# Optimization experiments

Measured on AMD Instinct MI355X. Metric: run time of the kernel, lower is better.

## Reference

```python
import jax, jax.numpy as jnp
import numpy as np

# Mamba2 config (matches mamba_ssm.Mamba2 defaults used by the wrapper)
D_MODEL = 1024
D_STATE = 128
D_CONV = 4
EXPAND = 2
HEADDIM = 64
CHUNK = 256
D_INNER = EXPAND * D_MODEL            # 2048
NHEADS = D_INNER // HEADDIM           # 32
CONV_DIM = D_INNER + 2 * D_STATE      # 2304 (x, B, C share the causal conv)
D_IN_PROJ = 2 * D_INNER + 2 * D_STATE + NHEADS  # z, xBC, dt
EPS = 1e-5


def rmsnorm(x, w, eps=EPS):
    return x * jax.lax.rsqrt(jnp.mean(x * x, axis=-1, keepdims=True) + eps) * w


def setup_inputs() -> dict:
    key = jax.random.key(0)
    ks = jax.random.split(key, 8)
    B, L = 2, 2048
    def w(k, shape, sc=0.02):
        return jax.random.normal(k, shape, jnp.float32) * sc
    return {
        "x": jax.random.normal(ks[0], (B, L, D_MODEL), jnp.float32),
        "norm_w": jnp.ones((D_MODEL,), jnp.float32),
        "in_proj_w": w(ks[1], (D_IN_PROJ, D_MODEL)),
        "conv_w": w(ks[2], (CONV_DIM, 1, D_CONV), 0.2),   # depthwise kernel
        "conv_b": jnp.zeros((CONV_DIM,), jnp.float32),
        "dt_bias": w(ks[3], (NHEADS,), 1.0),
        "A_log": jnp.log(1.0 + 15.0 * jax.random.uniform(ks[4], (NHEADS,), jnp.float32)),
        "D": jnp.ones((NHEADS,), jnp.float32),
        "gnorm_w": jnp.ones((D_INNER,), jnp.float32),
        "out_proj_w": w(ks[5], (D_MODEL, D_INNER)),
    }


def _ssd(xd, a, Bm, Cm):
    """Chunked SSD scan (ssd_minimal_discrete).
    xd: (b,l,h,p) = x*dt ; a: (b,l,h) = dt*A ; Bm,Cm: (b,l,n) (ngroups=1)."""
    b, l, h, p = xd.shape
    n = Bm.shape[-1]
    nc = l // CHUNK
    xd = xd.reshape(b, nc, CHUNK, h, p)
    a = a.reshape(b, nc, CHUNK, h).transpose(0, 3, 1, 2)   # (b,h,nc,c)
    Bm = Bm.reshape(b, nc, CHUNK, n)
    Cm = Cm.reshape(b, nc, CHUNK, n)
    a_cs = jnp.cumsum(a, axis=-1)                           # (b,h,nc,c)
    # 1) intra-chunk: causal decay matrix L[t,s] = exp(sum_{s<i<=t} a_i)
    diff = a_cs[..., :, None] - a_cs[..., None, :]          # (b,h,nc,c,c)
    mask = jnp.tril(jnp.ones((CHUNK, CHUNK), bool))
    Lm = jnp.exp(jnp.where(mask, diff, 0.0)) * mask
    Y_diag = jnp.einsum("bcln,bcsn,bhcls,bcshp->bclhp", Cm, Bm, Lm, xd)
    # 2) per-chunk end states
    decay_states = jnp.exp(a_cs[..., -1:] - a_cs)           # (b,h,nc,c)
    states = jnp.einsum("bcln,bhcl,bclhp->bchpn", Bm, decay_states, xd)
    # 3) inter-chunk recurrence (vectorized segsum over the 8+1 chunk totals)
    tot = jnp.pad(a_cs[..., -1], ((0, 0), (0, 0), (1, 0)))  # (b,h,nc+1)
    tot_cs = jnp.cumsum(tot, axis=-1)
    dchunk = tot_cs[..., :, None] - tot_cs[..., None, :]    # (b,h,nc+1,nc+1)
    cmask = jnp.tril(jnp.ones((nc + 1, nc + 1), bool))
    dchunk = jnp.exp(jnp.where(cmask, dchunk, 0.0)) * cmask
    states = jnp.concatenate([jnp.zeros_like(states[:, :1]), states], axis=1)
    new_states = jnp.einsum("bhzc,bchpn->bzhpn", dchunk, states)
    init_states = new_states[:, :-1]                        # state entering each chunk
    # 4) state -> output contribution
    Y_off = jnp.einsum("bcln,bchpn,bhcl->bclhp", Cm, init_states, jnp.exp(a_cs))
    return (Y_diag + Y_off).reshape(b, l, h, p)


def reference(x, norm_w, in_proj_w, conv_w, conv_b, dt_bias, A_log, D, gnorm_w, out_proj_w):
    res = x
    u = rmsnorm(x, norm_w)
    zxbcdt = u @ in_proj_w.T                                # (b,l,d_in_proj)
    z, xBC, dt = jnp.split(zxbcdt, [D_INNER, D_INNER + CONV_DIM], axis=-1)
    # causal depthwise conv1d over (x,B,C), then SiLU
    xBC_t = jnp.pad(xBC.transpose(0, 2, 1), ((0, 0), (0, 0), (D_CONV - 1, 0)))
    conv = jax.lax.conv_general_dilated(
        xBC_t, conv_w, (1,), "VALID",
        dimension_numbers=("NCH", "OIH", "NCH"), feature_group_count=CONV_DIM)
    xBC = jax.nn.silu(conv.transpose(0, 2, 1) + conv_b)
    xs, Bm, Cm = jnp.split(xBC, [D_INNER, D_INNER + D_STATE], axis=-1)
    dt = jax.nn.softplus(dt + dt_bias)                      # (b,l,h)
    A = -jnp.exp(A_log)                                     # (h,)
    xh = xs.reshape(xs.shape[0], xs.shape[1], NHEADS, HEADDIM)
    y = _ssd(xh * dt[..., None], dt * A, Bm, Cm)
    y = y + D[None, None, :, None] * xh                     # skip term
    y = y.reshape(xs.shape)
    y = rmsnorm(y * jax.nn.silu(z), gnorm_w)                # gated RMSNorm
    return res + y @ out_proj_w.T
```

## Files before the change

### kernel.cpp

```cpp
#include <hip/hip_runtime.h>
#include <hip/hip_bf16.h>

typedef __hip_bfloat16 bf16_t;
typedef __attribute__((ext_vector_type(8))) short bfrag8;
typedef __attribute__((ext_vector_type(4))) float floatx4;

#define DM     1024
#define DI     2048
#define NHD    32
#define HD     64
#define DSTATE 128
#define CONVD  2304
#define NPROJ  4384
#define NPAD   4480
#define MR     4096
#define LL     2048
#define EPSF   1e-5f
#define LOG2E  1.44269504088896f

__device__ __forceinline__ void gl_lds16(const void* g, void* l) {
  __builtin_amdgcn_global_load_lds((const __attribute__((address_space(1))) void*)g,
                                   (__attribute__((address_space(3))) void*)l, 16, 0, 0);
}
__device__ __forceinline__ unsigned pack_bf16_rn(float a, float b) {
  unsigned ua = (__float_as_uint(a) + 0x8000u) >> 16;
  unsigned ub = (__float_as_uint(b) + 0x8000u) >> 16;
  return ua | (ub << 16);
}
__device__ __forceinline__ unsigned short bf16u(float a) {
  return (unsigned short)((__float_as_uint(a) + 0x8000u) >> 16);
}
__device__ __forceinline__ float blo(unsigned u){ return __uint_as_float(u << 16); }
__device__ __forceinline__ float bhi(unsigned u){ return __uint_as_float(u & 0xffff0000u); }
__device__ __forceinline__ void unp8(uint4 u, float* v) {
  v[0]=blo(u.x); v[1]=bhi(u.x); v[2]=blo(u.y); v[3]=bhi(u.y);
  v[4]=blo(u.z); v[5]=bhi(u.z); v[6]=blo(u.w); v[7]=bhi(u.w);
}
typedef union { unsigned u[4]; bfrag8 f; } fragu;

#define W1CNT (NPAD * DM / 4)
#define W2CNT (DM * DI / 4)
#define CVTBLK ((W1CNT + W2CNT) / 256)
__global__ void rms_cvt_kernel(const float* __restrict__ x, const float* __restrict__ w,
                               bf16_t* __restrict__ ub,
                               const float* __restrict__ w1, const float* __restrict__ w2,
                               const float* __restrict__ gw,
                               bf16_t* __restrict__ o1, bf16_t* __restrict__ o2) {
  __shared__ float red[4];
  int t = threadIdx.x;
  if (blockIdx.x < MR) {
    int row = blockIdx.x;
    float4 v = ((const float4*)(x + (long)row * DM))[t];
    float ss = v.x*v.x + v.y*v.y + v.z*v.z + v.w*v.w;
#pragma unroll
    for (int off = 32; off > 0; off >>= 1) ss += __shfl_down(ss, off, 64);
    if ((t & 63) == 0) red[t >> 6] = ss;
    __syncthreads();
    float tot = red[0] + red[1] + red[2] + red[3];
    float rs = rsqrtf(tot * (1.f / DM) + EPSF);
    float4 wv = ((const float4*)w)[t];
    bf16_t* o = ub + (long)row * DM + t * 4;
    o[0] = __float2bfloat16(v.x * rs * wv.x);
    o[1] = __float2bfloat16(v.y * rs * wv.y);
    o[2] = __float2bfloat16(v.z * rs * wv.z);
    o[3] = __float2bfloat16(v.w * rs * wv.w);
  } else {
    int i4 = (blockIdx.x - MR) * 256 + t;
    if (i4 < W1CNT) {
      int idx = i4 * 4;
      int row = idx >> 10;
      float4 v = make_float4(0.f, 0.f, 0.f, 0.f);
      if (row < NPROJ) v = *(const float4*)(w1 + idx);
      bf16_t* d = o1 + idx;
      d[0] = __float2bfloat16(v.x); d[1] = __float2bfloat16(v.y);
      d[2] = __float2bfloat16(v.z); d[3] = __float2bfloat16(v.w);
    } else {
      int idx = (i4 - W1CNT) * 4;
      int k = idx & (DI - 1);
      float4 v = *(const float4*)(w2 + idx);
      float4 g = *(const float4*)(gw + k);
      bf16_t* d = o2 + idx;
      d[0] = __float2bfloat16(v.x * g.x); d[1] = __float2bfloat16(v.y * g.y);
      d[2] = __float2bfloat16(v.z * g.z); d[3] = __float2bfloat16(v.w * g.w);
    }
  }
}

template<int TN, bool DO_RES, bool OUT_BF16>
__global__ __launch_bounds__(256) void gemm64_kernel(const bf16_t* __restrict__ A,
    const bf16_t* __restrict__ Bw, const float* __restrict__ resid,
    const float* __restrict__ ssqp, void* __restrict__ Cout, int N, int K) {
  __shared__ bf16_t As[128 * 64];
  __shared__ bf16_t Bs[TN * 64];
  __shared__ float rsS[128];
  const int tid = threadIdx.x;
  const int lane = tid & 63;
  const int wv = tid >> 6;
  const int l15 = lane & 15;
  const int l4 = lane >> 4;
  constexpr int MF = (TN == 128) ? 4 : 2;
  const int wm = (TN == 128) ? ((wv >> 1) << 6) : (wv << 5);
  const int wn = (TN == 128) ? ((wv & 1) << 6) : 0;
  const int tm = blockIdx.x << 7;
  const int tn = blockIdx.y * TN;

  if (DO_RES) {
    int rr = tid >> 1;
    const float4* pp = (const float4*)(ssqp + (long)(tm + rr) * 32 + (tid & 1) * 16);
    float s = 0.f;
#pragma unroll
    for (int q = 0; q < 4; q++) { float4 v = pp[q]; s += v.x + v.y + v.z + v.w; }
    s += __shfl_xor(s, 1, 64);
    if ((tid & 1) == 0) rsS[rr] = rsqrtf(s * (1.f / DI) + EPSF);
  }

  floatx4 acc[MF][4];
#pragma unroll
  for (int i = 0; i < MF; i++)
#pragma unroll
    for (int j = 0; j < 4; j++) acc[i][j] = (floatx4){0.f, 0.f, 0.f, 0.f};

  const int r = tid >> 3;
  const int c8 = tid & 7;
  const int scol = ((c8 ^ (r & 7)) << 3);
  const bf16_t* Ag = A + (long)(tm + r) * K + scol;
  const bf16_t* Bg = Bw + (long)(tn + r) * K + scol;
  const int swz = l15 & 7;

  for (int k0 = 0; k0 < K; k0 += 64) {
#pragma unroll
    for (int q = 0; q < 4; q++)
      gl_lds16(Ag + (long)(q * 32) * K + k0, &As[q * 2048 + tid * 8]);
#pragma unroll
    for (int q = 0; q < TN / 32; q++)
      gl_lds16(Bg + (long)(q * 32) * K + k0, &Bs[q * 2048 + tid * 8]);
    __syncthreads();
#pragma unroll
    for (int kk = 0; kk < 2; kk++) {
      bfrag8 af[MF], bfr[4];
      const int ch = ((kk << 2) | l4) ^ swz;
#pragma unroll
      for (int j = 0; j < 4; j++)
        bfr[j] = *(const bfrag8*)&Bs[(wn + j * 16 + l15) * 64 + ch * 8];
#pragma unroll
      for (int i = 0; i < MF; i++)
        af[i] = *(const bfrag8*)&As[(wm + i * 16 + l15) * 64 + ch * 8];
#pragma unroll
      for (int i = 0; i < MF; i++)
#pragma unroll
        for (int j = 0; j < 4; j++)
          acc[i][j] = __builtin_amdgcn_mfma_f32_16x16x32_bf16(af[i], bfr[j], acc[i][j], 0, 0, 0);
    }
    __syncthreads();
  }
#pragma unroll
  for (int i = 0; i < MF; i++)
#pragma unroll
    for (int j = 0; j < 4; j++)
#pragma unroll
      for (int r2 = 0; r2 < 4; r2++) {
        int row = tm + wm + i * 16 + l4 * 4 + r2;
        int col = tn + wn + j * 16 + l15;
        float v = acc[i][j][r2];
        if (OUT_BF16) {
          ((bf16_t*)Cout)[(long)row * N + col] = __float2bfloat16(v);
        } else {
          if (DO_RES) v = v * rsS[row - tm] + resid[(long)row * N + col];
          ((float*)Cout)[(long)row * N + col] = v;
        }
      }
}

__global__ __launch_bounds__(512, 2) void gemm256_kernel(const bf16_t* __restrict__ A,
    const bf16_t* __restrict__ Bw, bf16_t* __restrict__ Cout) {
  __shared__ bf16_t lds[65536];
  const int t = threadIdx.x;
  const int lane = t & 63, wv = t >> 6;
  const int wm = wv >> 2, wn = wv & 3;
  const int l15 = lane & 15, l4 = lane >> 4;
  const int xcd = blockIdx.x & 7, idx = blockIdx.x >> 3;
  const int bx = (xcd & 3) * 4 + (idx & 3);
  const int by = (xcd >> 2) * 8 + (idx >> 2);
  const int tm = bx << 8, tn = by << 8;

  const int srow = t >> 3;
  const int scol = ((t & 7) ^ (srow & 7)) << 3;
  const bf16_t* Ag = A + (long)(tm + srow) * DM + scol;
  const bf16_t* Bg = Bw + (long)(tn + srow) * DM + scol;
  bf16_t* Asl = lds;
  bf16_t* Bsl = lds + 32768;
  const int swl = (l15 & 7) << 4;
  const int ca0 = (l4 * 16) ^ swl;
  const int ca1 = (64 + l4 * 16) ^ swl;

  floatx4 acc[8][4];
#pragma unroll
  for (int i = 0; i < 8; i++)
#pragma unroll
    for (int j = 0; j < 4; j++) acc[i][j] = (floatx4){0.f, 0.f, 0.f, 0.f};
  bfrag8 bq[8];

#define STG_A(tt, h) { \
  bf16_t* d_ = Asl + (((tt) & 1) * 2 + (h)) * 8192 + t * 8; \
  gl_lds16(Ag + (long)((h) * 128     ) * DM + (tt) * 64, d_); \
  gl_lds16(Ag + (long)((h) * 128 + 64) * DM + (tt) * 64, d_ + 4096); \
}
#define STG_B(tt, h) { \
  bf16_t* d_ = Bsl + (((tt) & 1) * 2 + (h)) * 8192 + t * 8; \
  gl_lds16(Bg + (long)((h) * 128     ) * DM + (tt) * 64, d_); \
  gl_lds16(Bg + (long)((h) * 128 + 64) * DM + (tt) * 64, d_ + 4096); \
}
#define PH(d, q, STG, WT) { \
  const char* Ah_ = (const char*)(Asl + ((d) * 2 + wm) * 8192); \
  const char* Bh_ = (const char*)(Bsl + ((d) * 2 + (wn >> 1)) * 8192); \
  if ((q) == 0) { \
    _Pragma("unroll") \
    for (int j = 0; j < 4; j++) { \
      int r_ = ((wn & 1) << 6) + j * 16 + l15; \
      bq[j * 2]     = *(const bfrag8*)(Bh_ + r_ * 128 + ca0); \
      bq[j * 2 + 1] = *(const bfrag8*)(Bh_ + r_ * 128 + ca1); \
    } \
  } \
  bfrag8 aq0, aq1, aq2, aq3; \
  { int r_ = (q) * 32 + l15; \
    aq0 = *(const bfrag8*)(Ah_ + r_ * 128 + ca0); \
    aq1 = *(const bfrag8*)(Ah_ + r_ * 128 + ca1); \
    aq2 = *(const bfrag8*)(Ah_ + (r_ + 16) * 128 + ca0); \
    aq3 = *(const bfrag8*)(Ah_ + (r_ + 16) * 128 + ca1); } \
  STG; \
  __builtin_amdgcn_s_barrier(); \
  asm volatile("s_waitcnt lgkmcnt(0)" ::: "memory"); \
  __builtin_amdgcn_s_setprio(1); \
  _Pragma("unroll") \
  for (int j = 0; j < 4; j++) { \
    acc[(q)*2  ][j] = __builtin_amdgcn_mfma_f32_16x16x32_bf16(aq0, bq[j*2],   acc[(q)*2  ][j], 0, 0, 0); \
    acc[(q)*2  ][j] = __builtin_amdgcn_mfma_f32_16x16x32_bf16(aq1, bq[j*2+1], acc[(q)*2  ][j], 0, 0, 0); \
    acc[(q)*2+1][j] = __builtin_amdgcn_mfma_f32_16x16x32_bf16(aq2, bq[j*2],   acc[(q)*2+1][j], 0, 0, 0); \
    acc[(q)*2+1][j] = __builtin_amdgcn_mfma_f32_16x16x32_bf16(aq3, bq[j*2+1], acc[(q)*2+1][j], 0, 0, 0); \
  } \
  __builtin_amdgcn_s_setprio(0); \
  WT; \
  __builtin_amdgcn_s_barrier(); \
}

  STG_A(0, 0); STG_A(0, 1); STG_B(0, 0); STG_B(0, 1);
  STG_B(1, 0); STG_B(1, 1);
  asm volatile("s_waitcnt vmcnt(4)" ::: "memory");
  __builtin_amdgcn_s_barrier();

  for (int it = 0; it < 7; ++it) {
    const int ta = 2 * it, tb = ta + 1;
    PH(0, 0, STG_A(tb, 0), {})
    PH(0, 1, STG_A(tb, 1), {})
    PH(0, 2, STG_B(ta + 2, 0), {})
    PH(0, 3, STG_B(ta + 2, 1), asm volatile("s_waitcnt vmcnt(4)" ::: "memory");)
    PH(1, 0, STG_A(ta + 2, 0), {})
    PH(1, 1, STG_A(ta + 2, 1), {})
    PH(1, 2, STG_B(tb + 2, 0), {})
    PH(1, 3, STG_B(tb + 2, 1), asm volatile("s_waitcnt vmcnt(4)" ::: "memory");)
  }
  {
    PH(0, 0, STG_A(15, 0), {})
    PH(0, 1, STG_A(15, 1), {})
    PH(0, 2, {}, {})
    PH(0, 3, {}, asm volatile("s_waitcnt vmcnt(0)" ::: "memory");)
    PH(1, 0, {}, {})
    PH(1, 1, {}, {})
    PH(1, 2, {}, {})
    PH(1, 3, {}, {})
  }
#undef PH
#undef STG_A
#undef STG_B

  const long crow = tm + wm * 128;
  const int ccol = tn + wn * 64;
#pragma unroll
  for (int qi = 0; qi < 8; qi++)
#pragma unroll
    for (int j = 0; j < 4; j++)
#pragma unroll
      for (int r2 = 0; r2 < 4; r2++) {
        long row = crow + (qi >> 1) * 32 + (qi & 1) * 16 + l4 * 4 + r2;
        int col = ccol + j * 16 + l15;
        Cout[row * NPAD + col] = __float2bfloat16(acc[qi][j][r2]);
      }
}

__global__ __launch_bounds__(256) void sst_kernel(const bf16_t* __restrict__ xdTe,
    const bf16_t* __restrict__ BmT, bf16_t* __restrict__ states,
    const bf16_t* __restrict__ Cmh, const bf16_t* __restrict__ Bmh,
    float* __restrict__ SL) {
  __shared__ bf16_t As[128 * 32];
  __shared__ bf16_t Bs[128 * 32];
  const int t = threadIdx.x, lane = t & 63, wv = t >> 6;
  const int l15 = lane & 15, l4 = lane >> 4;
  if (blockIdx.x < 512) {
    int blk = blockIdx.x;
    int bc = blk >> 5;
    floatx4 acc[2][4];
#pragma unroll
    for (int i = 0; i < 2; i++)
#pragma unroll
      for (int j = 0; j < 4; j++) acc[i][j] = (floatx4){0.f, 0.f, 0.f, 0.f};
    const bf16_t* arow = BmT + (long)bc * 128 * 256;
    const bf16_t* brow = xdTe + (long)blk * 64 * 256;
#pragma unroll
    for (int kt = 0; kt < 8; kt++) {
      bfrag8 af[2], bfr[4];
#pragma unroll
      for (int i = 0; i < 2; i++)
        af[i] = *(const bfrag8*)(arow + (long)(wv * 32 + i * 16 + l15) * 256 + kt * 32 + l4 * 8);
#pragma unroll
      for (int j = 0; j < 4; j++)
        bfr[j] = *(const bfrag8*)(brow + (long)(j * 16 + l15) * 256 + kt * 32 + l4 * 8);
#pragma unroll
      for (int i = 0; i < 2; i++)
#pragma unroll
        for (int j = 0; j < 4; j++)
          acc[i][j] = __builtin_amdgcn_mfma_f32_16x16x32_bf16(af[i], bfr[j], acc[i][j], 0, 0, 0);
    }
#pragma unroll
    for (int i = 0; i < 2; i++)
#pragma unroll
      for (int j = 0; j < 4; j++) {
        int n_base = wv * 32 + i * 16 + l4 * 4;
        int p = j * 16 + l15;
        unsigned lo = pack_bf16_rn(acc[i][j][0], acc[i][j][1]);
        unsigned hi = pack_bf16_rn(acc[i][j][2], acc[i][j][3]);
        *(uint2*)(states + (long)blk * 8192 + p * 128 + n_base) = make_uint2(lo, hi);
      }
  } else {
    int idx = blockIdx.x - 512;
    const int bc = idx >> 2;
    const int tm = ((idx >> 1) & 1) << 7;
    const int tn = (idx & 1) << 7;
    const int wm = (wv >> 1) << 6;
    const int wn = (wv & 1) << 6;
    floatx4 acc[4][4];
#pragma unroll
    for (int i = 0; i < 4; i++)
#pragma unroll
      for (int j = 0; j < 4; j++) acc[i][j] = (floatx4){0.f, 0.f, 0.f, 0.f};
    const int arow = t >> 2;
    const int acol = (t & 3) << 3;
    const bf16_t* Ag = Cmh + (long)bc * 256 * DSTATE + (long)(tm + arow) * DSTATE + acol;
    const bf16_t* Bg = Bmh + (long)bc * 256 * DSTATE + (long)(tn + arow) * DSTATE + acol;
    const long k64 = (long)64 * DSTATE;
    for (int k0 = 0; k0 < DSTATE; k0 += 32) {
      gl_lds16(Ag + k0, &As[t * 8]);
      gl_lds16(Ag + k64 + k0, &As[2048 + t * 8]);
      gl_lds16(Bg + k0, &Bs[t * 8]);
      gl_lds16(Bg + k64 + k0, &Bs[2048 + t * 8]);
      __syncthreads();
      bfrag8 af[4], bfr[4];
#pragma unroll
      for (int i = 0; i < 4; i++)
        af[i] = *(const bfrag8*)&As[(wm + i * 16 + l15) * 32 + l4 * 8];
#pragma unroll
      for (int j = 0; j < 4; j++)
        bfr[j] = *(const bfrag8*)&Bs[(wn + j * 16 + l15) * 32 + l4 * 8];
#pragma unroll
      for (int i = 0; i < 4; i++)
#pragma unroll
        for (int j = 0; j < 4; j++)
          acc[i][j] = __builtin_amdgcn_mfma_f32_16x16x32_bf16(af[i], bfr[j], acc[i][j], 0, 0, 0);
      __syncthreads();
    }
    float* Cb = SL + (long)bc * 65536;
#pragma unroll
    for (int i = 0; i < 4; i++)
#pragma unroll
      for (int j = 0; j < 4; j++)
#pragma unroll
        for (int r = 0; r < 4; r++)
          Cb[(long)(tm + wm + i * 16 + l4 * 4 + r) * 256 + tn + wn + j * 16 + l15] = acc[i][j][r];
  }
}

__global__ __launch_bounds__(256) void conv4_kernel(const bf16_t* __restrict__ zxh,
    const float* __restrict__ cw, const float* __restrict__ cb,
    bf16_t* __restrict__ xhb, bf16_t* __restrict__ Bmh, bf16_t* __restrict__ Cmh) {
  int g = blockIdx.x * 256 + threadIdx.x;
  int cg = g % 288;
  int blt = g / 288;
  int c0 = cg * 8;
  long bl0 = (long)blt * 4;
  int l0 = (int)(bl0 & (LL - 1));
  const bf16_t* base = zxh + bl0 * NPAD + DI + c0;
  float rv[7][8];
#pragma unroll
  for (int j = 0; j < 7; j++) {
    int dj = j - 3;
    if (l0 + dj >= 0) {
      uint4 u = *(const uint4*)(base + (long)dj * NPAD);
      unp8(u, rv[j]);
    } else {
#pragma unroll
      for (int q = 0; q < 8; q++) rv[j][q] = 0.f;
    }
  }
  float4 wq[8];
#pragma unroll
  for (int q = 0; q < 8; q++) wq[q] = ((const float4*)cw)[c0 + q];
  float bias[8];
  *(float4*)&bias[0] = *(const float4*)(cb + c0);
  *(float4*)&bias[4] = *(const float4*)(cb + c0 + 4);
#pragma unroll
  for (int i = 0; i < 4; i++) {
    unsigned o[4];
#pragma unroll
    for (int q2 = 0; q2 < 4; q2++) {
      float rr[2];
#pragma unroll
      for (int e = 0; e < 2; e++) {
        int q = q2 * 2 + e;
        float a = bias[q] + wq[q].x * rv[i][q] + wq[q].y * rv[i + 1][q]
                + wq[q].z * rv[i + 2][q] + wq[q].w * rv[i + 3][q];
        rr[e] = a / (1.f + __expf(-a));
      }
      o[q2] = pack_bf16_rn(rr[0], rr[1]);
    }
    uint4 ov = make_uint4(o[0], o[1], o[2], o[3]);
    long bl = bl0 + i;
    if (c0 < DI)               *(uint4*)(xhb + bl * DI + c0) = ov;
    else if (c0 < DI + DSTATE) *(uint4*)(Bmh + bl * DSTATE + (c0 - DI)) = ov;
    else                       *(uint4*)(Cmh + bl * DSTATE + (c0 - DI - DSTATE)) = ov;
  }
}

__global__ __launch_bounds__(256) void xdt_kernel(const bf16_t* __restrict__ xhb,
    const bf16_t* __restrict__ Bmh, const bf16_t* __restrict__ zxh,
    const float* __restrict__ A_log, const float* __restrict__ dtb,
    float* __restrict__ acs, float* __restrict__ ctot,
    bf16_t* __restrict__ xdT, bf16_t* __restrict__ xdTe, bf16_t* __restrict__ BmT) {
  __shared__ unsigned short Tb[9216];
  __shared__ float acsL[256];
  __shared__ float dtsL[256];
  __shared__ float wsum[4];
  int blk = blockIdx.x;
  int t = threadIdx.x;
  if (blk < 512) {
    int h = blk & 31, bc = blk >> 5;
    {
      int lane = t & 63, w = t >> 6;
      float Ah = -__expf(A_log[h]) * LOG2E;
      int gl = bc * 256 + t;
      float vv = __bfloat162float(zxh[(long)gl * NPAD + (NPROJ - 32) + h]) + dtb[h];
      float sp = fmaxf(vv, 0.f) + log1pf(__expf(-fabsf(vv)));
      float a = sp * Ah;
#pragma unroll
      for (int off = 1; off < 64; off <<= 1) {
        float v = __shfl_up(a, off, 64);
        if (lane >= off) a += v;
      }
      if (lane == 63) wsum[w] = a;
      __syncthreads();
      float base = 0.f;
      for (int i = 0; i < 4; i++) base += (i < w) ? wsum[i] : 0.f;
      a += base;
      acsL[t] = a;
      dtsL[t] = sp;
      acs[blk * 256 + t] = a;
      if (t == 255) ctot[blk] = a;
      __syncthreads();
    }
    float atot = acsL[255];
    unsigned short* T1 = Tb;
    unsigned short* T2 = Tb + 4608;
    int l_loc = t >> 2, pg = t & 3;
    for (int lt = 0; lt < 4; lt++) {
      int ll = lt * 64 + l_loc;
      int gl = bc * 256 + ll;
      float w1 = dtsL[ll];
      float w2 = w1 * exp2f(atot - acsL[ll]);
      const uint4* src = (const uint4*)(xhb + (long)gl * DI + h * HD + pg * 16);
      uint4 u0 = src[0], u1 = src[1];
      float v[16];
      unp8(u0, v); unp8(u1, v + 8);
      __syncthreads();
#pragma unroll
      for (int q = 0; q < 16; q++) {
        T1[(pg * 16 + q) * 72 + l_loc] = bf16u(v[q] * w1);
        T2[(pg * 16 + q) * 72 + l_loc] = bf16u(v[q] * w2);
      }
      __syncthreads();
      long orow = ((long)blk * 64 + l_loc) * 256 + lt * 64 + pg * 16;
      *(uint4*)(xdT + orow)      = *(uint4*)&T1[l_loc * 72 + pg * 16];
      *(uint4*)(xdT + orow + 8)  = *(uint4*)&T1[l_loc * 72 + pg * 16 + 8];
      *(uint4*)(xdTe + orow)     = *(uint4*)&T2[l_loc * 72 + pg * 16];
      *(uint4*)(xdTe + orow + 8) = *(uint4*)&T2[l_loc * 72 + pg * 16 + 8];
    }
  } else {
    unsigned short* T = Tb;
    int bc = blk - 512;
    int l_loc = t >> 2, ng = t & 3;
    for (int lt = 0; lt < 4; lt++) {
      int gl = bc * 256 + lt * 64 + l_loc;
      const uint4* src = (const uint4*)(Bmh + (long)gl * DSTATE + ng * 32);
      uint4 u[4];
#pragma unroll
      for (int q = 0; q < 4; q++) u[q] = src[q];
      __syncthreads();
      const unsigned short* us = (const unsigned short*)u;
#pragma unroll
      for (int e = 0; e < 32; e++)
        T[(ng * 32 + e) * 72 + l_loc] = us[e];
      __syncthreads();
      int n = t >> 1, lg2 = t & 1;
      long orow = ((long)bc * 128 + n) * 256 + lt * 64 + lg2 * 32;
#pragma unroll
      for (int q = 0; q < 4; q++)
        *(uint4*)(BmT + orow + q * 8) = *(uint4*)&T[n * 72 + lg2 * 32 + q * 8];
    }
  }
}

__global__ void scan_kernel(const bf16_t* __restrict__ states, const float* __restrict__ ctot,
                            bf16_t* __restrict__ initsb) {
  int id = blockIdx.x * 256 + threadIdx.x;
  int pn = id & 8191;
  int bh = id >> 13;
  int b = bh >> 5, h = bh & 31;
  float S = 0.f;
#pragma unroll
  for (int c = 0; c < 8; c++) {
    int blk = (b * 8 + c) * 32 + h;
    initsb[(long)blk * 8192 + pn] = __float2bfloat16(S);
    S = exp2f(ctot[blk]) * S + __bfloat162float(states[(long)blk * 8192 + pn]);
  }
}

__global__ __launch_bounds__(512, 4) void yk4_kernel(const float* __restrict__ SL,
     const bf16_t* __restrict__ Cmh, const bf16_t* __restrict__ xhb,
     const bf16_t* __restrict__ zxh, const float* __restrict__ acs,
     const bf16_t* __restrict__ initsb, const bf16_t* __restrict__ xdT,
     const float* __restrict__ Dp, bf16_t* __restrict__ yg, float* __restrict__ ssqp) {
  int bi = blockIdx.x;
  int bc = (bi & 7) * 2 + ((bi >> 3) & 1);
  int h = bi >> 4;
  int ablk = bc * 32 + h;
  int t = threadIdx.x;
  int wv = t >> 6;
  int mh = wv >> 2, wsub = wv & 3;
  int lane = t & 63;
  int l15 = lane & 15, l4 = lane >> 4;

  __shared__ float acsS[256];
  __shared__ __align__(16) char bbuf[49152];
  bf16_t* xds = (bf16_t*)bbuf;
  bf16_t* ins = (bf16_t*)(bbuf + 32768);
  float* Yt = (float*)bbuf;

  {
    const bf16_t* xrow_g = xdT + (long)ablk * 64 * 256;
#pragma unroll
    for (int it = 0; it < 4; it++) {
      int sl = it * 512 + t;
      int p = sl >> 5, s = sl & 31;
      int c = (s & 24) | ((s & 7) ^ (p & 7));
      gl_lds16(xrow_g + p * 256 + c * 8, &xds[sl * 8]);
    }
    const bf16_t* irow_g = initsb + (long)ablk * 8192;
#pragma unroll
    for (int it = 0; it < 2; it++) {
      int sl = it * 512 + t;
      int p = sl >> 4, s = sl & 15;
      int c = (s & 8) | ((s & 7) ^ (p & 7));
      gl_lds16(irow_g + p * 128 + c * 8, &ins[sl * 8]);
    }
  }
  if (t < 256) acsS[t] = acs[ablk * 256 + t];
  __syncthreads();

  const int rowbase = bc * 256;
  const int l0 = mh * 128 + wsub * 32 + l15;
  const int l1 = l0 + 16;
  const float al0 = acsS[l0], al1 = acsS[l1];
  const float eA0 = exp2f(al0), eA1 = exp2f(al1);
  const float* SL0 = SL + (long)bc * 65536 + (long)l0 * 256;
  const float* SL1 = SL + (long)bc * 65536 + (long)l1 * 256;

  floatx4 acc[2][4];
#pragma unroll
  for (int i = 0; i < 2; i++)
#pragma unroll
    for (int j = 0; j < 4; j++) acc[i][j] = (floatx4){0.f, 0.f, 0.f, 0.f};

  const int nkd = (mh + 1) * 4;
  for (int kt = 0; kt < nkd; kt++) {
    int sbase = kt * 32 + l4 * 8;
    float as[8];
    *(float4*)&as[0] = *(const float4*)&acsS[sbase];
    *(float4*)&as[4] = *(const float4*)&acsS[sbase + 4];
    float sv0[8], sv1[8];
    *(float4*)&sv0[0] = *(const float4*)(SL0 + sbase);
    *(float4*)&sv0[4] = *(const float4*)(SL0 + sbase + 4);
    *(float4*)&sv1[0] = *(const float4*)(SL1 + sbase);
    *(float4*)&sv1[4] = *(const float4*)(SL1 + sbase + 4);
    fragu af0, af1;
#pragma unroll
    for (int q2 = 0; q2 < 4; q2++) {
      float p00, p01, p10, p11;
      {
        int s = sbase + q2 * 2;
        float d0 = al0 - as[q2 * 2], d1 = al0 - as[q2 * 2 + 1];
        p00 = (s <= l0) ? sv0[q2 * 2] * exp2f(fminf(d0, 0.f)) : 0.f;
        p01 = (s + 1 <= l0) ? sv0[q2 * 2 + 1] * exp2f(fminf(d1, 0.f)) : 0.f;
        float e0 = al1 - as[q2 * 2], e1 = al1 - as[q2 * 2 + 1];
        p10 = (s <= l1) ? sv1[q2 * 2] * exp2f(fminf(e0, 0.f)) : 0.f;
        p11 = (s + 1 <= l1) ? sv1[q2 * 2 + 1] * exp2f(fminf(e1, 0.f)) : 0.f;
      }
      af0.u[q2] = pack_bf16_rn(p00, p01);
      af1.u[q2] = pack_bf16_rn(p10, p11);
    }
    bfrag8 bfr[4];
    int ch = kt * 4 + l4;
#pragma unroll
    for (int j = 0; j < 4; j++) {
      int p = j * 16 + l15;
      int sw = (ch & 24) | ((ch & 7) ^ (p & 7));
      bfr[j] = *(const bfrag8*)&xds[(p * 32 + sw) * 8];
    }
#pragma unroll
    for (int j = 0; j < 4; j++) {
      acc[0][j] = __builtin_amdgcn_mfma_f32_16x16x32_bf16(af0.f, bfr[j], acc[0][j], 0, 0, 0);
      acc[1][j] = __builtin_amdgcn_mfma_f32_16x16x32_bf16(af1.f, bfr[j], acc[1][j], 0, 0, 0);
    }
  }
#pragma unroll
  for (int kt = 0; kt < 4; kt++) {
    int n0 = kt * 32 + l4 * 8;
    uint4 c0 = *(const uint4*)(Cmh + (long)(rowbase + l0) * DSTATE + n0);
    uint4 c1 = *(const uint4*)(Cmh + (long)(rowbase + l1) * DSTATE + n0);
    float cv0[8], cv1[8];
    unp8(c0, cv0); unp8(c1, cv1);
    fragu af0, af1;
#pragma unroll
    for (int q2 = 0; q2 < 4; q2++) {
      af0.u[q2] = pack_bf16_rn(cv0[q2 * 2] * eA0, cv0[q2 * 2 + 1] * eA0);
      af1.u[q2] = pack_bf16_rn(cv1[q2 * 2] * eA1, cv1[q2 * 2 + 1] * eA1);
    }
    bfrag8 bfr[4];
    int ch = kt * 4 + l4;
#pragma unroll
    for (int j = 0; j < 4; j++) {
      int p = j * 16 + l15;
      int sw = (ch & 8) | ((ch & 7) ^ (p & 7));
      bfr[j] = *(const bfrag8*)&ins[(p * 16 + sw) * 8];
    }
#pragma unroll
    for (int j = 0; j < 4; j++) {
      acc[0][j] = __builtin_amdgcn_mfma_f32_16x16x32_bf16(af0.f, bfr[j], acc[0][j], 0, 0, 0);
      acc[1][j] = __builtin_amdgcn_mfma_f32_16x16x32_bf16(af1.f, bfr[j], acc[1][j], 0, 0, 0);
    }
  }
  float Dh = Dp[h];
#pragma unroll
  for (int pass = 0; pass < 2; pass++) {
    __syncthreads();
    if (mh == pass) {
#pragma unroll
      for (int i = 0; i < 2; i++)
#pragma unroll
        for (int j = 0; j < 4; j++)
#pragma unroll
          for (int r = 0; r < 4; r++)
            Yt[(wsub * 32 + i * 16 + l4 * 4 + r) * 66 + j * 16 + l15] = acc[i][j][r];
    }
    __syncthreads();
    {
      int row_l = t >> 2;
      int chc = (t & 3) * 16;
      long rowg = rowbase + pass * 128 + row_l;
      float ss = 0.f;
#pragma unroll
      for (int it = 0; it < 2; it++) {
        int c = chc + it * 8;
        float4 y0 = *(const float4*)&Yt[row_l * 66 + c];
        float4 y1 = *(const float4*)&Yt[row_l * 66 + c + 4];
        uint4 ux = *(const uint4*)(xhb + rowg * DI + h * HD + c);
        uint4 uz = *(const uint4*)(zxh + rowg * NPAD + h * HD + c);
        float xv[8], zv[8];
        unp8(ux, xv); unp8(uz, zv);
        float yv[8] = {y0.x, y0.y, y0.z, y0.w, y1.x, y1.y, y1.z, y1.w};
        unsigned o[4];
#pragma unroll
        for (int q = 0; q < 4; q++) {
          float v0 = (yv[q * 2 + 0] + Dh * xv[q * 2 + 0]) *
                     (zv[q * 2 + 0] / (1.f + __expf(-zv[q * 2 + 0])));
          float v1 = (yv[q * 2 + 1] + Dh * xv[q * 2 + 1]) *
                     (zv[q * 2 + 1] / (1.f + __expf(-zv[q * 2 + 1])));
          ss += v0 * v0 + v1 * v1;
          o[q] = pack_bf16_rn(v0, v1);
        }
        *(uint4*)(yg + rowg * DI + h * HD + c) = make_uint4(o[0], o[1], o[2], o[3]);
      }
      ss += __shfl_xor(ss, 1, 64);
      ss += __shfl_xor(ss, 2, 64);
      if ((t & 3) == 0) ssqp[rowg * 32 + h] = ss;
    }
  }
}

extern "C" void kernel_launch(void* const* d_in, const int* in_sizes, int n_in,
                              void* d_out, int out_size, void* d_ws, size_t ws_size,
                              hipStream_t stream) {
  const float* x    = (const float*)d_in[0];
  const float* nw   = (const float*)d_in[1];
  const float* w1   = (const float*)d_in[2];
  const float* cw   = (const float*)d_in[3];
  const float* cb   = (const float*)d_in[4];
  const float* dtb  = (const float*)d_in[5];
  const float* alog = (const float*)d_in[6];
  const float* Dp   = (const float*)d_in[7];
  const float* gw   = (const float*)d_in[8];
  const float* w2   = (const float*)d_in[9];
  float* out = (float*)d_out;

  char* ws = (char*)d_ws;
  size_t off = 0;
  auto alloc = [&](size_t bytes) -> void* {
    void* p = ws + off;
    off += (bytes + 255) & ~(size_t)255;
    return p;
  };
  bf16_t* ub     = (bf16_t*)alloc((size_t)MR * DM * 2);
  bf16_t* w1b    = (bf16_t*)alloc((size_t)NPAD * DM * 2);
  bf16_t* w2b    = (bf16_t*)alloc((size_t)DM * DI * 2);
  bf16_t* zxh    = (bf16_t*)alloc((size_t)MR * NPAD * 2);
  bf16_t* xhb    = (bf16_t*)alloc((size_t)MR * DI * 2);
  bf16_t* Bmh    = (bf16_t*)alloc((size_t)MR * DSTATE * 2);
  bf16_t* Cmh    = (bf16_t*)alloc((size_t)MR * DSTATE * 2);
  float* SL      = (float*)alloc((size_t)16 * 256 * 256 * 4);
  float* acs     = (float*)alloc((size_t)512 * 256 * 4);
  float* ctot    = (float*)alloc((size_t)512 * 4);
  bf16_t* states = (bf16_t*)alloc((size_t)512 * 8192 * 2);
  bf16_t* initsb = (bf16_t*)alloc((size_t)512 * 8192 * 2);
  bf16_t* xdT    = (bf16_t*)alloc((size_t)512 * 64 * 256 * 2);
  bf16_t* xdTe   = (bf16_t*)alloc((size_t)512 * 64 * 256 * 2);
  bf16_t* BmT    = (bf16_t*)alloc((size_t)16 * 128 * 256 * 2);
  bf16_t* yg     = (bf16_t*)alloc((size_t)MR * DI * 2);
  float* ssqp    = (float*)alloc((size_t)MR * NHD * 4);
  if (off > ws_size) return;

  rms_cvt_kernel<<<MR + CVTBLK, 256, 0, stream>>>(x, nw, ub, w1, w2, gw, w1b, w2b);
  gemm256_kernel<<<256, 512, 0, stream>>>(ub, w1b, zxh);
  gemm64_kernel<64, false, true><<<dim3(MR / 128, 6), 256, 0, stream>>>(
      ub, w1b + (size_t)4096 * DM, nullptr, nullptr, zxh + 4096, NPAD, DM);
  conv4_kernel<<<(1024 * 288) / 256, 256, 0, stream>>>(zxh, cw, cb, xhb, Bmh, Cmh);
  xdt_kernel<<<528, 256, 0, stream>>>(xhb, Bmh, zxh, alog, dtb, acs, ctot, xdT, xdTe, BmT);
  sst_kernel<<<576, 256, 0, stream>>>(xdTe, BmT, states, Cmh, Bmh, SL);
  scan_kernel<<<(2 * 32 * 8192) / 256, 256, 0, stream>>>(states, ctot, initsb);
  yk4_kernel<<<512, 512, 0, stream>>>(SL, Cmh, xhb, zxh, acs, initsb, xdT, Dp, yg, ssqp);
  gemm64_kernel<64, true, false><<<dim3(MR / 128, DM / 64), 256, 0, stream>>>(
      yg, w2b, x, ssqp, out, DM, DI);
}
```

Measured before the change: 258.7 us.

## Fuse in_proj tail GEMM into main GEMM launch and store SL in bf16

Adds 96 extra blocks to the 256x256 in_proj GEMM kernel that compute the leftover 384 columns (4096..4479) with a 128x64-per-half tiling, removing the separate gemm64 launch and letting the tail run alongside the main tiles. It also changes the intra-chunk CB^T score matrix SL from fp32 to bf16, halving its write traffic in sst and read traffic in yk4. The risks are lower precision of the score matrix before the decay is applied, and load imbalance from the tail blocks sharing the grid.

```diff
diff --git a/kernel.cpp b/kernel.cpp
--- a/kernel.cpp
+++ b/kernel.cpp
@@ -175,6 +175,71 @@
     const bf16_t* __restrict__ Bw, bf16_t* __restrict__ Cout) {
   __shared__ bf16_t lds[65536];
   const int t = threadIdx.x;
+
+  if (blockIdx.x >= 256) {
+    const int idx = blockIdx.x - 256;
+    const int mi = idx & 15, ni = idx >> 4;
+    const int hh = t >> 8;
+    const int tl = t & 255;
+    const int lane = tl & 63, wv = tl >> 6;
+    const int l15 = lane & 15, l4 = lane >> 4;
+    const int wm = wv << 5;
+    const int tm = mi * 256 + hh * 128;
+    const int tn = 4096 + ni * 64;
+    bf16_t* As = lds + hh * 8192;
+    bf16_t* Bs = lds + 16384;
+    floatx4 acc[2][4];
+#pragma unroll
+    for (int i = 0; i < 2; i++)
+#pragma unroll
+      for (int j = 0; j < 4; j++) acc[i][j] = (floatx4){0.f, 0.f, 0.f, 0.f};
+    const int r = tl >> 3;
+    const int c8 = tl & 7;
+    const int scol = ((c8 ^ (r & 7)) << 3);
+    const bf16_t* Ag = A + (long)(tm + r) * DM + scol;
+    const bf16_t* Bg = Bw + (long)(tn + r) * DM + scol;
+    const int swz = l15 & 7;
+    for (int k0 = 0; k0 < DM; k0 += 64) {
+#pragma unroll
+      for (int q = 0; q < 4; q++)
+        gl_lds16(Ag + (long)(q * 32) * DM + k0, &As[q * 2048 + tl * 8]);
+      if (hh == 0) {
+#pragma unroll
+        for (int q = 0; q < 2; q++)
+          gl_lds16(Bg + (long)(q * 32) * DM + k0, &Bs[q * 2048 + tl * 8]);
+      }
+      __syncthreads();
+#pragma unroll
+      for (int kk = 0; kk < 2; kk++) {
+        bfrag8 af[2], bfr[4];
+        const int ch = ((kk << 2) | l4) ^ swz;
+#pragma unroll
+        for (int j = 0; j < 4; j++)
+          bfr[j] = *(const bfrag8*)&Bs[(j * 16 + l15) * 64 + ch * 8];
+#pragma unroll
+        for (int i = 0; i < 2; i++)
+          af[i] = *(const bfrag8*)&As[(wm + i * 16 + l15) * 64 + ch * 8];
+#pragma unroll
+        for (int i = 0; i < 2; i++)
+#pragma unroll
+          for (int j = 0; j < 4; j++)
+            acc[i][j] = __builtin_amdgcn_mfma_f32_16x16x32_bf16(af[i], bfr[j], acc[i][j], 0, 0, 0);
+      }
+      __syncthreads();
+    }
+#pragma unroll
+    for (int i = 0; i < 2; i++)
+#pragma unroll
+      for (int j = 0; j < 4; j++)
+#pragma unroll
+        for (int r2 = 0; r2 < 4; r2++) {
+          int row = tm + wm + i * 16 + l4 * 4 + r2;
+          int col = tn + j * 16 + l15;
+          Cout[(long)row * NPAD + col] = __float2bfloat16(acc[i][j][r2]);
+        }
+    return;
+  }
+
   const int lane = t & 63, wv = t >> 6;
   const int wm = wv >> 2, wn = wv & 3;
   const int l15 = lane & 15, l4 = lane >> 4;
@@ -290,7 +355,7 @@
 __global__ __launch_bounds__(256) void sst_kernel(const bf16_t* __restrict__ xdTe,
     const bf16_t* __restrict__ BmT, bf16_t* __restrict__ states,
     const bf16_t* __restrict__ Cmh, const bf16_t* __restrict__ Bmh,
-    float* __restrict__ SL) {
+    bf16_t* __restrict__ SL) {
   __shared__ bf16_t As[128 * 32];
   __shared__ bf16_t Bs[128 * 32];
   const int t = threadIdx.x, lane = t & 63, wv = t >> 6;
@@ -367,14 +432,15 @@
           acc[i][j] = __builtin_amdgcn_mfma_f32_16x16x32_bf16(af[i], bfr[j], acc[i][j], 0, 0, 0);
       __syncthreads();
     }
-    float* Cb = SL + (long)bc * 65536;
+    bf16_t* Cb = SL + (long)bc * 65536;
 #pragma unroll
     for (int i = 0; i < 4; i++)
 #pragma unroll
       for (int j = 0; j < 4; j++)
 #pragma unroll
         for (int r = 0; r < 4; r++)
-          Cb[(long)(tm + wm + i * 16 + l4 * 4 + r) * 256 + tn + wn + j * 16 + l15] = acc[i][j][r];
+          Cb[(long)(tm + wm + i * 16 + l4 * 4 + r) * 256 + tn + wn + j * 16 + l15] =
+              __float2bfloat16(acc[i][j][r]);
   }
 }
 
@@ -531,7 +597,7 @@
   }
 }
 
-__global__ __launch_bounds__(512, 4) void yk4_kernel(const float* __restrict__ SL,
+__global__ __launch_bounds__(512, 4) void yk4_kernel(const bf16_t* __restrict__ SL,
      const bf16_t* __restrict__ Cmh, const bf16_t* __restrict__ xhb,
      const bf16_t* __restrict__ zxh, const float* __restrict__ acs,
      const bf16_t* __restrict__ initsb, const bf16_t* __restrict__ xdT,
@@ -578,8 +644,8 @@
   const int l1 = l0 + 16;
   const float al0 = acsS[l0], al1 = acsS[l1];
   const float eA0 = exp2f(al0), eA1 = exp2f(al1);
-  const float* SL0 = SL + (long)bc * 65536 + (long)l0 * 256;
-  const float* SL1 = SL + (long)bc * 65536 + (long)l1 * 256;
+  const bf16_t* SL0 = SL + (long)bc * 65536 + (long)l0 * 256;
+  const bf16_t* SL1 = SL + (long)bc * 65536 + (long)l1 * 256;
 
   floatx4 acc[2][4];
 #pragma unroll
@@ -594,10 +660,8 @@
     *(float4*)&as[0] = *(const float4*)&acsS[sbase];
     *(float4*)&as[4] = *(const float4*)&acsS[sbase + 4];
     float sv0[8], sv1[8];
-    *(float4*)&sv0[0] = *(const float4*)(SL0 + sbase);
-    *(float4*)&sv0[4] = *(const float4*)(SL0 + sbase + 4);
-    *(float4*)&sv1[0] = *(const float4*)(SL1 + sbase);
-    *(float4*)&sv1[4] = *(const float4*)(SL1 + sbase + 4);
+    unp8(*(const uint4*)(SL0 + sbase), sv0);
+    unp8(*(const uint4*)(SL1 + sbase), sv1);
     fragu af0, af1;
 #pragma unroll
     for (int q2 = 0; q2 < 4; q2++) {
@@ -732,7 +796,7 @@
   bf16_t* xhb    = (bf16_t*)alloc((size_t)MR * DI * 2);
   bf16_t* Bmh    = (bf16_t*)alloc((size_t)MR * DSTATE * 2);
   bf16_t* Cmh    = (bf16_t*)alloc((size_t)MR * DSTATE * 2);
-  float* SL      = (float*)alloc((size_t)16 * 256 * 256 * 4);
+  bf16_t* SL     = (bf16_t*)alloc((size_t)16 * 256 * 256 * 2);
   float* acs     = (float*)alloc((size_t)512 * 256 * 4);
   float* ctot    = (float*)alloc((size_t)512 * 4);
   bf16_t* states = (bf16_t*)alloc((size_t)512 * 8192 * 2);
@@ -745,9 +809,7 @@
   if (off > ws_size) return;
 
   rms_cvt_kernel<<<MR + CVTBLK, 256, 0, stream>>>(x, nw, ub, w1, w2, gw, w1b, w2b);
-  gemm256_kernel<<<256, 512, 0, stream>>>(ub, w1b, zxh);
-  gemm64_kernel<64, false, true><<<dim3(MR / 128, 6), 256, 0, stream>>>(
-      ub, w1b + (size_t)4096 * DM, nullptr, nullptr, zxh + 4096, NPAD, DM);
+  gemm256_kernel<<<352, 512, 0, stream>>>(ub, w1b, zxh);
   conv4_kernel<<<(1024 * 288) / 256, 256, 0, stream>>>(zxh, cw, cb, xhb, Bmh, Cmh);
   xdt_kernel<<<528, 256, 0, stream>>>(xhb, Bmh, zxh, alog, dtb, acs, ctot, xdT, xdTe, BmT);
   sst_kernel<<<576, 256, 0, stream>>>(xdTe, BmT, states, Cmh, Bmh, SL);
```

Result: faster. 250.5 us (-3.2%).
